# Optimization experiments

Measured on AMD Instinct MI355X. Metric: run time of the kernel, lower is better.

The kernel has to match this reference:

```python
import jax, jax.numpy as jnp
import numpy as np

NEG_INF = -jnp.inf


def setup_inputs() -> dict:
    key = jax.random.key(0)
    ks = jax.random.split(key, 6)
    B, S, D, DK = 8, 2048, 1024, 128
    x = jax.random.normal(ks[0], (B, S, D), dtype=jnp.float32)
    context = jax.random.normal(ks[1], (B, S, D), dtype=jnp.float32)
    # torch nn.Linear weights: [out_features, in_features]
    Wq = jax.random.normal(ks[2], (DK, D), dtype=jnp.float32) * 0.02
    Wk = jax.random.normal(ks[3], (DK, D), dtype=jnp.float32) * 0.02
    Wv = jax.random.normal(ks[4], (DK, D), dtype=jnp.float32) * 0.02
    # valid lengths in [S//2, S] so every row has at least one valid key
    batch_lengths = jax.random.randint(ks[5], (B,), S // 2, S + 1, dtype=jnp.int32)
    return {
        "x": x,
        "context": context,
        "Wq": Wq,
        "Wk": Wk,
        "Wv": Wv,
        "batch_lengths": batch_lengths,
        "max_len": S,
        "decoding": 1,
    }


def reference(x, context, Wq, Wk, Wv, batch_lengths, max_len, decoding):
    B, S, D = x.shape
    dk = Wq.shape[0]
    pos = jnp.arange(S)
    # outputMask: 1.0 for t < length, else 0.0; broadcast over feature dim dk
    valid = pos[None, :] < batch_lengths[:, None]            # [B, S]
    mask = valid[:, :, None].astype(x.dtype)                 # [B, S, 1] (broadcast to dk)
    Q = jnp.einsum('bsd,kd->bsk', context, Wq) * mask        # [B, S, dk]
    K = jnp.einsum('bsd,kd->bsk', context, Wk) * mask
    V = jnp.einsum('bsd,kd->bsk', x, Wv) * mask
    energy = jnp.einsum('bqk,bjk->bqj', Q, K)                # [B, S, S]
    # attnMask: -inf at padded key positions (j >= length)
    key_pad = ~valid                                         # [B, S]
    energy = jnp.where(key_pad[:, None, :], NEG_INF, energy)
    if decoding:
        # causal: energy[:, i, j] = -inf for j > i (the python double loop)
        causal = pos[:, None] < pos[None, :]                 # [S, S], True above diag
        energy = jnp.where(causal[None, :, :], NEG_INF, energy)
    score = jax.nn.softmax(energy / jnp.sqrt(jnp.asarray(dk, x.dtype)), axis=-1)
    return jnp.einsum('bqj,bjk->bqk', score, V)              # [B, S, dk]
```

## Files before the change

### kernel.cpp

```cpp
#include <hip/hip_runtime.h>
#include <hip/hip_bf16.h>

#define BB 8
#define SS 2048
#define DD 1024
#define DKK 128
#define N_ITEMS 4608

using bf16x8  = __attribute__((ext_vector_type(8))) __bf16;
using floatx4 = __attribute__((ext_vector_type(4))) float;
using intx4   = __attribute__((ext_vector_type(4))) int;

__device__ __forceinline__ void lds16(const void* g, void* l) {
    __builtin_amdgcn_global_load_lds((const __attribute__((address_space(1))) void*)g,
                                     (__attribute__((address_space(3))) void*)l, 16, 0, 0);
}

__device__ __forceinline__ int pack2(float a, float b) {
    union { __bf16 h; unsigned short u; } ua, ub;
    ua.h = (__bf16)a; ub.h = (__bf16)b;
    return (int)(ua.u | ((unsigned)ub.u << 16));
}

__global__ __launch_bounds__(256) void convw_kernel(
    const float* __restrict__ Wq, const float* __restrict__ Wk,
    const float* __restrict__ Wv, __bf16* __restrict__ Wt)
{
    const int z = blockIdx.y;
    const float* W = (z == 0) ? Wq : (z == 1) ? Wk : Wv;
    const int t  = blockIdx.x * 256 + threadIdx.x;
    const int n  = t >> 7;
    const int k0 = (t & 127) * 8;
    float4 f0 = *(const float4*)(W + n * DD + k0);
    float4 f1 = *(const float4*)(W + n * DD + k0 + 4);
    bf16x8 v;
    v[0]=(__bf16)f0.x; v[1]=(__bf16)f0.y; v[2]=(__bf16)f0.z; v[3]=(__bf16)f0.w;
    v[4]=(__bf16)f1.x; v[5]=(__bf16)f1.y; v[6]=(__bf16)f1.z; v[7]=(__bf16)f1.w;
    const int kb  = (k0 >> 3) & 7;
    const int kbs = kb ^ (n & 7);
    *(bf16x8*)(Wt + (size_t)z * 131072 + ((k0 >> 6) * 128 + n) * 64 + kbs * 8) = v;
}

__global__ __launch_bounds__(256, 2) void proj_kernel(
    const float* __restrict__ x, const float* __restrict__ ctx,
    const __bf16* __restrict__ Wt, const int* __restrict__ lengths,
    __bf16* __restrict__ Qb, __bf16* __restrict__ Kb, __bf16* __restrict__ Vt)
{
    __shared__ __align__(16) __bf16 SH[20992];
    __bf16* Abuf = SH;
    __bf16* Wl0  = SH + 4608;
    __bf16* Wl1  = SH + 12800;
    __bf16* T    = SH + 4608;

    const int isV = blockIdx.x >= 256;
    const int m0  = (isV ? blockIdx.x - 256 : blockIdx.x) * 64;
    const int b   = m0 >> 11;
    const int s0  = m0 & (SS - 1);
    const int len = lengths[b];
    if (s0 >= len) return;

    const int tid  = threadIdx.x;
    const int wave = tid >> 6;
    const int lane = tid & 63;
    const int quad = lane >> 4;
    const int l16  = lane & 15;
    const int wm   = wave >> 1;
    const int wn   = wave & 1;

    const float*  A  = isV ? x : ctx;
    const __bf16* W0 = isV ? (Wt + 262144) : Wt;
    const __bf16* W1 = Wt + 131072;

    const int r    = tid >> 2;
    const int kseg = (tid & 3) * 16;
    const float* Ab = A + (size_t)(m0 + r) * DD + kseg;

    floatx4 acc[2][2][4];
#pragma unroll
    for (int m_ = 0; m_ < 2; ++m_)
#pragma unroll
        for (int i = 0; i < 2; ++i)
#pragma unroll
            for (int j = 0; j < 4; ++j) acc[m_][i][j] = (floatx4){0.f,0.f,0.f,0.f};

    float4 pf[4];
#pragma unroll
    for (int i = 0; i < 4; ++i) pf[i] = *(const float4*)(Ab + i * 4);

    for (int t = 0; t < 16; ++t) {
        __syncthreads();
        {
            bf16x8 c0, c1;
            c0[0]=(__bf16)pf[0].x; c0[1]=(__bf16)pf[0].y; c0[2]=(__bf16)pf[0].z; c0[3]=(__bf16)pf[0].w;
            c0[4]=(__bf16)pf[1].x; c0[5]=(__bf16)pf[1].y; c0[6]=(__bf16)pf[1].z; c0[7]=(__bf16)pf[1].w;
            c1[0]=(__bf16)pf[2].x; c1[1]=(__bf16)pf[2].y; c1[2]=(__bf16)pf[2].z; c1[3]=(__bf16)pf[2].w;
            c1[4]=(__bf16)pf[3].x; c1[5]=(__bf16)pf[3].y; c1[6]=(__bf16)pf[3].z; c1[7]=(__bf16)pf[3].w;
            *(bf16x8*)&Abuf[r * 72 + kseg]     = c0;
            *(bf16x8*)&Abuf[r * 72 + kseg + 8] = c1;
        }
#pragma unroll
        for (int i = 0; i < 4; ++i) {
            const int c = wave * 4 + i;
            lds16(W0 + (size_t)t * 8192 + c * 512 + lane * 8, Wl0 + c * 512);
            if (!isV)
                lds16(W1 + (size_t)t * 8192 + c * 512 + lane * 8, Wl1 + c * 512);
        }
        if (t < 15) {
            const float* ap = Ab + (t + 1) * 64;
#pragma unroll
            for (int i = 0; i < 4; ++i) pf[i] = *(const float4*)(ap + i * 4);
        }
        __syncthreads();

#pragma unroll
        for (int kh = 0; kh < 2; ++kh) {
            bf16x8 af[2];
#pragma unroll
            for (int mt = 0; mt < 2; ++mt)
                af[mt] = *(const bf16x8*)&Abuf[(wm*32 + mt*16 + l16) * 72 + kh*32 + quad*8];
            const int kb = kh * 4 + quad;
#pragma unroll
            for (int nt = 0; nt < 4; ++nt) {
                const int n = wn * 64 + nt * 16 + l16;
                const int off = n * 64 + ((kb ^ (n & 7)) << 3);
                bf16x8 w0 = *(const bf16x8*)&Wl0[off];
#pragma unroll
                for (int mt = 0; mt < 2; ++mt)
                    acc[0][mt][nt] = __builtin_amdgcn_mfma_f32_16x16x32_bf16(af[mt], w0, acc[0][mt][nt], 0, 0, 0);
                if (!isV) {
                    bf16x8 w1 = *(const bf16x8*)&Wl1[off];
#pragma unroll
                    for (int mt = 0; mt < 2; ++mt)
                        acc[1][mt][nt] = __builtin_amdgcn_mfma_f32_16x16x32_bf16(af[mt], w1, acc[1][mt][nt], 0, 0, 0);
                }
            }
        }
    }

    if (!isV) {
#pragma unroll
        for (int mt = 0; mt < 2; ++mt)
#pragma unroll
            for (int rr = 0; rr < 4; ++rr) {
                const int row = m0 + wm*32 + mt*16 + quad*4 + rr;
                const float mk = ((row & (SS - 1)) < len) ? 1.f : 0.f;
#pragma unroll
                for (int nt = 0; nt < 4; ++nt) {
                    const int col = wn*64 + nt*16 + l16;
                    Qb[(size_t)row * DKK + col] = (__bf16)(acc[0][mt][nt][rr] * mk);
                    Kb[(size_t)row * DKK + col] = (__bf16)(acc[1][mt][nt][rr] * mk);
                }
            }
    } else {
        __syncthreads();
#pragma unroll
        for (int mt = 0; mt < 2; ++mt)
#pragma unroll
            for (int nt = 0; nt < 4; ++nt)
#pragma unroll
                for (int rr = 0; rr < 4; ++rr) {
                    const int s = wm*32 + mt*16 + quad*4 + rr;
                    const int n = wn*64 + nt*16 + l16;
                    const float mk = (s0 + s < len) ? 1.f : 0.f;
                    T[n * 72 + s] = (__bf16)(acc[0][mt][nt][rr] * mk);
                }
        __syncthreads();
        const int n = tid >> 1, h = tid & 1;
        __bf16* dst = Vt + (size_t)b * DKK * SS + (size_t)n * SS + s0 + h * 32;
#pragma unroll
        for (int i = 0; i < 4; ++i)
            *(bf16x8*)(dst + i * 8) = *(const bf16x8*)&T[n * 72 + h * 32 + i * 8];
    }
}

__global__ __launch_bounds__(256) void vmean_kernel(
    const __bf16* __restrict__ Vt, const int* __restrict__ lengths,
    float* __restrict__ Vmean)
{
    const int b   = blockIdx.x >> 3;
    const int g3  = blockIdx.x & 7;
    const int len = lengths[b];
    const int tid = threadIdx.x;
    const int n   = g3 * 16 + (tid >> 4);
    const int sl  = (tid & 15) * 128;
    const __bf16* src = Vt + (size_t)b * DKK * SS + (size_t)n * SS + sl;
    float s = 0.f;
#pragma unroll
    for (int i = 0; i < 16; ++i) {
        bf16x8 v = *(const bf16x8*)(src + i * 8);
#pragma unroll
        for (int j = 0; j < 8; ++j)
            s += (sl + i * 8 + j < len) ? (float)v[j] : 0.f;
    }
#pragma unroll
    for (int off = 1; off < 16; off <<= 1)
        s += __shfl_xor(s, off, 64);
    if ((tid & 15) == 0) Vmean[b * DKK + n] = s / (float)len;
}

__global__ __launch_bounds__(64) void attn_part_kernel(
    const __bf16* __restrict__ Qb, const __bf16* __restrict__ Kb,
    const __bf16* __restrict__ Vt, const int* __restrict__ lengths,
    float* __restrict__ Oacc, float* __restrict__ Lacc)
{
    const int f = blockIdx.x;
    const int b = f / 576;
    const int r = f - b * 576;
    int a = (int)((sqrtf((float)(4 * (r >> 3) + 1)) - 1.0f) * 0.5f);
    while (8 * (a + 1) * (a + 2) <= r) ++a;
    while (8 * a * (a + 1) > r) --a;
    const int rp = r - 8 * a * (a + 1);
    const int dt = rp / (a + 1);
    const int c  = rp - dt * (a + 1);
    const int t  = 16 * a + dt;

    const int qw  = t * 16;
    const int len = lengths[b];
    if (qw >= len) return;
    const int jmax = min(qw + 16, len);
    const int jlo  = c * 256;
    if (jlo >= jmax) return;
    const int jhi = min(jlo + 256, jmax);

    const int lane = threadIdx.x;
    const int quad = lane >> 4;
    const int l16  = lane & 15;

    const __bf16* Qbase = Qb + (size_t)(b * SS + qw) * DKK;
    const __bf16* Kbase = Kb + (size_t)b * SS * DKK;
    const __bf16* Vbase = Vt + (size_t)b * DKK * SS;

    bf16x8 qfrag[4];
#pragma unroll
    for (int cc = 0; cc < 4; ++cc)
        qfrag[cc] = *(const bf16x8*)(Qbase + (size_t)l16 * DKK + cc * 32 + quad * 8);

    floatx4 oacc[8];
#pragma unroll
    for (int nt = 0; nt < 8; ++nt) oacc[nt] = (floatx4){0.f,0.f,0.f,0.f};
    float lsum = 0.f;
    const float scale = 0.08838834764831845f;
    const int   iq    = qw + l16;

    for (int j0 = jlo; j0 < jhi; j0 += 32) {
        bf16x8 kf[2][4];
#pragma unroll
        for (int jt = 0; jt < 2; ++jt)
#pragma unroll
            for (int cc = 0; cc < 4; ++cc)
                kf[jt][cc] = *(const bf16x8*)(
                    Kbase + (size_t)(j0 + jt*16 + l16) * DKK + cc*32 + quad*8);
        bf16x8 vf[8];
#pragma unroll
        for (int nt = 0; nt < 8; ++nt)
            vf[nt] = *(const bf16x8*)(Vbase + (size_t)(nt*16 + l16) * SS + j0 + quad*8);

        floatx4 st[2];
#pragma unroll
        for (int jt = 0; jt < 2; ++jt) {
            st[jt] = (floatx4){0.f,0.f,0.f,0.f};
#pragma unroll
            for (int cc = 0; cc < 4; ++cc)
                st[jt] = __builtin_amdgcn_mfma_f32_16x16x32_bf16(
                    kf[jt][cc], qfrag[cc], st[jt], 0, 0, 0);
        }
        int pk[2][2];
#pragma unroll
        for (int jt = 0; jt < 2; ++jt) {
            float p[4];
#pragma unroll
            for (int rr = 0; rr < 4; ++rr) {
                const int j = j0 + jt*16 + quad*4 + rr;
                p[rr] = (j > iq || j >= len) ? 0.f : __expf(st[jt][rr] * scale - 8.f);
                lsum += p[rr];
            }
            pk[jt][0] = pack2(p[0], p[1]);
            pk[jt][1] = pack2(p[2], p[3]);
        }
        const int a0 = (((quad & 1) << 5) + l16) << 2;
        const int a1 = a0 + 64;
        const int r00 = __builtin_amdgcn_ds_bpermute(a0, pk[0][0]);
        const int r01 = __builtin_amdgcn_ds_bpermute(a0, pk[0][1]);
        const int r02 = __builtin_amdgcn_ds_bpermute(a0, pk[1][0]);
        const int r03 = __builtin_amdgcn_ds_bpermute(a0, pk[1][1]);
        const int r10 = __builtin_amdgcn_ds_bpermute(a1, pk[0][0]);
        const int r11 = __builtin_amdgcn_ds_bpermute(a1, pk[0][1]);
        const int r12 = __builtin_amdgcn_ds_bpermute(a1, pk[1][0]);
        const int r13 = __builtin_amdgcn_ds_bpermute(a1, pk[1][1]);
        const bool hi = quad >= 2;
        union { intx4 i; bf16x8 h; } u;
        u.i = (intx4){ hi ? r02 : r00, hi ? r03 : r01,
                       hi ? r12 : r10, hi ? r13 : r11 };
#pragma unroll
        for (int nt = 0; nt < 8; ++nt)
            oacc[nt] = __builtin_amdgcn_mfma_f32_16x16x32_bf16(u.h, vf[nt], oacc[nt], 0, 0, 0);
    }

    lsum += __shfl_xor(lsum, 16, 64);
    lsum += __shfl_xor(lsum, 32, 64);
    const int tile = b * 128 + t;
    if (lane < 16) atomicAdd(&Lacc[tile * 16 + l16], lsum);
#pragma unroll
    for (int nt = 0; nt < 8; ++nt)
#pragma unroll
        for (int rr = 0; rr < 4; ++rr)
            atomicAdd(&Oacc[(size_t)tile * 2048 + (quad*4 + rr) * 128 + nt*16 + l16],
                      oacc[nt][rr]);
}

__global__ __launch_bounds__(256) void attn_fin_kernel(
    const float* __restrict__ Oacc, const float* __restrict__ Lacc,
    const int* __restrict__ lengths, const float* __restrict__ Vmean,
    float* __restrict__ out)
{
    const int tile = blockIdx.x;
    const int b    = tile >> 7;
    const int qw   = (tile & 127) * 16;
    const int row  = threadIdx.x >> 4;
    const int c8   = (threadIdx.x & 15) * 8;
    float* op = out + (size_t)(b * SS + qw + row) * DKK + c8;

    if (qw >= lengths[b]) {
#pragma unroll
        for (int k = 0; k < 8; ++k) op[k] = Vmean[b * DKK + c8 + k];
        return;
    }
    const float inv = 1.f / Lacc[tile * 16 + row];
    const float4 o0 = *(const float4*)(Oacc + (size_t)tile * 2048 + row * 128 + c8);
    const float4 o1 = *(const float4*)(Oacc + (size_t)tile * 2048 + row * 128 + c8 + 4);
    op[0] = o0.x*inv; op[1] = o0.y*inv; op[2] = o0.z*inv; op[3] = o0.w*inv;
    op[4] = o1.x*inv; op[5] = o1.y*inv; op[6] = o1.z*inv; op[7] = o1.w*inv;
}

extern "C" void kernel_launch(void* const* d_in, const int* in_sizes, int n_in,
                              void* d_out, int out_size, void* d_ws, size_t ws_size,
                              hipStream_t stream) {
    const float* x   = (const float*)d_in[0];
    const float* ctx = (const float*)d_in[1];
    const float* Wq  = (const float*)d_in[2];
    const float* Wk  = (const float*)d_in[3];
    const float* Wv  = (const float*)d_in[4];
    const int* lengths = (const int*)d_in[5];
    float* out = (float*)d_out;

    char* ws = (char*)d_ws;
    __bf16* Wt = (__bf16*)ws;
    __bf16* Qb = (__bf16*)(ws + 786432);
    __bf16* Kb = (__bf16*)(ws + 786432 + 4194304);
    __bf16* Vt = (__bf16*)(ws + 786432 + 8388608);
    float*  Vm = (float*) (ws + 786432 + 12582912);
    float*  Oa = (float*) (ws + 786432 + 12582912 + 4096);
    float*  La = (float*) (ws + 786432 + 12582912 + 4096 + 8388608);

    hipMemsetAsync(Oa, 0, 8388608 + 65536, stream);
    convw_kernel<<<dim3(64, 3), 256, 0, stream>>>(Wq, Wk, Wv, Wt);
    proj_kernel<<<512, 256, 0, stream>>>(x, ctx, Wt, lengths, Qb, Kb, Vt);
    vmean_kernel<<<64, 256, 0, stream>>>(Vt, lengths, Vm);
    attn_part_kernel<<<N_ITEMS, 64, 0, stream>>>(Qb, Kb, Vt, lengths, Oa, La);
    attn_fin_kernel<<<1024, 256, 0, stream>>>(Oa, La, lengths, Vm, out);
}
```

Before: 220.8 us.

## Replace split-K atomic attention with one block per query tile and K prefetch

Drops the split-key decomposition that used atomics into an fp32 accumulator, its memset and its separate finalize kernel. Each 64-thread block now handles one 16-row query tile over the whole key range, heaviest tiles first, and normalizes directly into the output. K fragments are double-buffered in registers so the next chunk's loads overlap the current chunk's compute. The trade-off is far less parallelism: 1024 single-wave blocks with up to 2048 keys each, so the longest tiles may dominate and leave compute units underused.

```diff
diff --git a/kernel.cpp b/kernel.cpp
--- a/kernel.cpp
+++ b/kernel.cpp
@@ -5,7 +5,6 @@
 #define SS 2048
 #define DD 1024
 #define DKK 128
-#define N_ITEMS 4608
 
 using bf16x8  = __attribute__((ext_vector_type(8))) __bf16;
 using floatx4 = __attribute__((ext_vector_type(4))) float;
@@ -198,34 +197,31 @@
     if ((tid & 15) == 0) Vmean[b * DKK + n] = s / (float)len;
 }
 
-__global__ __launch_bounds__(64) void attn_part_kernel(
+__global__ __launch_bounds__(64) void attn_kernel(
     const __bf16* __restrict__ Qb, const __bf16* __restrict__ Kb,
     const __bf16* __restrict__ Vt, const int* __restrict__ lengths,
-    float* __restrict__ Oacc, float* __restrict__ Lacc)
+    const float* __restrict__ Vmean, float* __restrict__ out)
 {
-    const int f = blockIdx.x;
-    const int b = f / 576;
-    const int r = f - b * 576;
-    int a = (int)((sqrtf((float)(4 * (r >> 3) + 1)) - 1.0f) * 0.5f);
-    while (8 * (a + 1) * (a + 2) <= r) ++a;
-    while (8 * a * (a + 1) > r) --a;
-    const int rp = r - 8 * a * (a + 1);
-    const int dt = rp / (a + 1);
-    const int c  = rp - dt * (a + 1);
-    const int t  = 16 * a + dt;
-
-    const int qw  = t * 16;
-    const int len = lengths[b];
-    if (qw >= len) return;
-    const int jmax = min(qw + 16, len);
-    const int jlo  = c * 256;
-    if (jlo >= jmax) return;
-    const int jhi = min(jlo + 256, jmax);
-
+    const int b    = blockIdx.x & 7;
+    const int t    = 127 - (blockIdx.x >> 3);
+    const int qw   = t * 16;
+    const int len  = lengths[b];
     const int lane = threadIdx.x;
     const int quad = lane >> 4;
     const int l16  = lane & 15;
 
+    if (qw >= len) {
+        const float4 v0 = *(const float4*)(Vmean + b * DKK + l16 * 8);
+        const float4 v1 = *(const float4*)(Vmean + b * DKK + l16 * 8 + 4);
+#pragma unroll
+        for (int rr = 0; rr < 4; ++rr) {
+            float* p = out + (size_t)(b * SS + qw + quad * 4 + rr) * DKK + l16 * 8;
+            *(float4*)p = v0; *(float4*)(p + 4) = v1;
+        }
+        return;
+    }
+
+    const int jmax = min(qw + 16, len);
     const __bf16* Qbase = Qb + (size_t)(b * SS + qw) * DKK;
     const __bf16* Kbase = Kb + (size_t)b * SS * DKK;
     const __bf16* Vbase = Vt + (size_t)b * DKK * SS;
@@ -242,14 +238,15 @@
     const float scale = 0.08838834764831845f;
     const int   iq    = qw + l16;
 
-    for (int j0 = jlo; j0 < jhi; j0 += 32) {
-        bf16x8 kf[2][4];
+    auto loadK = [&](bf16x8 (&kf)[2][4], int j0) {
 #pragma unroll
         for (int jt = 0; jt < 2; ++jt)
 #pragma unroll
             for (int cc = 0; cc < 4; ++cc)
                 kf[jt][cc] = *(const bf16x8*)(
                     Kbase + (size_t)(j0 + jt*16 + l16) * DKK + cc*32 + quad*8);
+    };
+    auto process = [&](const bf16x8 (&kf)[2][4], int j0) {
         bf16x8 vf[8];
 #pragma unroll
         for (int nt = 0; nt < 8; ++nt)
@@ -294,42 +291,36 @@
 #pragma unroll
         for (int nt = 0; nt < 8; ++nt)
             oacc[nt] = __builtin_amdgcn_mfma_f32_16x16x32_bf16(u.h, vf[nt], oacc[nt], 0, 0, 0);
+    };
+
+    bf16x8 kfA[2][4], kfB[2][4];
+    loadK(kfA, 0);
+    int j0 = 0;
+    while (true) {
+        bool more = (j0 + 32 < jmax);
+        if (more) loadK(kfB, j0 + 32);
+        process(kfA, j0);
+        j0 += 32;
+        if (!more) break;
+        more = (j0 + 32 < jmax);
+        if (more) loadK(kfA, j0 + 32);
+        process(kfB, j0);
+        j0 += 32;
+        if (!more) break;
     }
 
     lsum += __shfl_xor(lsum, 16, 64);
     lsum += __shfl_xor(lsum, 32, 64);
-    const int tile = b * 128 + t;
-    if (lane < 16) atomicAdd(&Lacc[tile * 16 + l16], lsum);
+    float inv[4];
+#pragma unroll
+    for (int rr = 0; rr < 4; ++rr)
+        inv[rr] = 1.f / __shfl(lsum, quad * 4 + rr, 64);
 #pragma unroll
     for (int nt = 0; nt < 8; ++nt)
 #pragma unroll
         for (int rr = 0; rr < 4; ++rr)
-            atomicAdd(&Oacc[(size_t)tile * 2048 + (quad*4 + rr) * 128 + nt*16 + l16],
-                      oacc[nt][rr]);
-}
-
-__global__ __launch_bounds__(256) void attn_fin_kernel(
-    const float* __restrict__ Oacc, const float* __restrict__ Lacc,
-    const int* __restrict__ lengths, const float* __restrict__ Vmean,
-    float* __restrict__ out)
-{
-    const int tile = blockIdx.x;
-    const int b    = tile >> 7;
-    const int qw   = (tile & 127) * 16;
-    const int row  = threadIdx.x >> 4;
-    const int c8   = (threadIdx.x & 15) * 8;
-    float* op = out + (size_t)(b * SS + qw + row) * DKK + c8;
-
-    if (qw >= lengths[b]) {
-#pragma unroll
-        for (int k = 0; k < 8; ++k) op[k] = Vmean[b * DKK + c8 + k];
-        return;
-    }
-    const float inv = 1.f / Lacc[tile * 16 + row];
-    const float4 o0 = *(const float4*)(Oacc + (size_t)tile * 2048 + row * 128 + c8);
-    const float4 o1 = *(const float4*)(Oacc + (size_t)tile * 2048 + row * 128 + c8 + 4);
-    op[0] = o0.x*inv; op[1] = o0.y*inv; op[2] = o0.z*inv; op[3] = o0.w*inv;
-    op[4] = o1.x*inv; op[5] = o1.y*inv; op[6] = o1.z*inv; op[7] = o1.w*inv;
+            out[(size_t)(b * SS + qw + quad*4 + rr) * DKK + nt*16 + l16] =
+                oacc[nt][rr] * inv[rr];
 }
 
 extern "C" void kernel_launch(void* const* d_in, const int* in_sizes, int n_in,
@@ -349,13 +340,9 @@
     __bf16* Kb = (__bf16*)(ws + 786432 + 4194304);
     __bf16* Vt = (__bf16*)(ws + 786432 + 8388608);
     float*  Vm = (float*) (ws + 786432 + 12582912);
-    float*  Oa = (float*) (ws + 786432 + 12582912 + 4096);
-    float*  La = (float*) (ws + 786432 + 12582912 + 4096 + 8388608);
-
-    hipMemsetAsync(Oa, 0, 8388608 + 65536, stream);
+
     convw_kernel<<<dim3(64, 3), 256, 0, stream>>>(Wq, Wk, Wv, Wt);
     proj_kernel<<<512, 256, 0, stream>>>(x, ctx, Wt, lengths, Qb, Kb, Vt);
     vmean_kernel<<<64, 256, 0, stream>>>(Vt, lengths, Vm);
-    attn_part_kernel<<<N_ITEMS, 64, 0, stream>>>(Qb, Kb, Vt, lengths, Oa, La);
-    attn_fin_kernel<<<1024, 256, 0, stream>>>(Oa, La, lengths, Vm, out);
-}
+    attn_kernel<<<1024, 64, 0, stream>>>(Qb, Kb, Vt, lengths, Vm, out);
+}
```

Result: slower. 237.1 us (+7.4%).
